# Kernel tuning notes

Hardware: AMD Instinct MI355X
Metric: run time of the kernel (lower is better)

## Reference

```python
import math
import jax, jax.numpy as jnp
import numpy as np

B, D, E, R, TOP_K = 16384, 2048, 64, 128, 2
TAU = 1.0
CAP_FACTOR = 1.25
TOP_C = min(E, max(4, 2 * TOP_K))  # GatingNetwork default top_c


def setup_inputs() -> dict:
    key = jax.random.key(0)
    ks = jax.random.split(key, 7)
    x = jax.random.normal(ks[0], (B, D), dtype=jnp.float32)
    # shared_encoder: nn.Linear(d, d) -> weight [out, in], bias [out]
    We = jax.random.normal(ks[1], (D, D), dtype=jnp.float32) / np.sqrt(D)
    be = jnp.zeros((D,), dtype=jnp.float32)
    # gating: nn.Linear(d, E, bias=False) -> weight [E, d]
    Wg = jax.random.normal(ks[2], (E, D), dtype=jnp.float32) / np.sqrt(D)
    # LowRankExpert per expert: U [r, d], V [d, r], gamma scalar (init 1.0)
    U = jax.random.normal(ks[3], (E, R, D), dtype=jnp.float32) / np.sqrt(D)
    V = jax.random.normal(ks[4], (E, D, R), dtype=jnp.float32) / np.sqrt(R)
    gamma = jnp.ones((E,), dtype=jnp.float32)
    return {"x": x, "We": We, "be": be, "Wg": Wg, "U": U, "V": V, "gamma": gamma}


def reference(x, We, be, Wg, U, V, gamma):
    # shared encoder
    enc = x @ We.T + be  # [B, D]

    # ---- gating: top-C candidates then top-K routing ----
    logits = (enc @ Wg.T) / TAU  # [B, E]
    topc_vals, topc_idx = jax.lax.top_k(logits, TOP_C)          # [B, C]
    topk_vals, pos_in_c = jax.lax.top_k(topc_vals, TOP_K)       # [B, K]
    topk_idx = jnp.take_along_axis(topc_idx, pos_in_c, axis=1)  # [B, K]
    # masked stable softmax over the K selected logits (with 1e-12 eps as in source)
    m = jnp.max(topk_vals, axis=-1, keepdims=True)
    ex = jnp.exp(topk_vals - m)
    w = ex / (jnp.sum(ex, axis=-1, keepdims=True) + 1e-12)      # [B, K]

    # ---- flatten assignments ----
    N = B * TOP_K
    tok = jnp.repeat(jnp.arange(B), TOP_K)   # [N]
    eid = topk_idx.reshape(-1)               # [N]
    wf = w.reshape(-1)                       # [N]
    wmask = wf > 1e-12

    # ---- capacity-based dispatch (sort/group equivalent, fixed shapes) ----
    cap = int(math.ceil(CAP_FACTOR * N / E))  # expert capacity
    onehot = ((eid[:, None] == jnp.arange(E)[None, :]) & wmask[:, None]).astype(jnp.int32)  # [N, E]
    pos = jnp.cumsum(onehot, axis=0) - onehot                      # position within expert
    pos_of = jnp.take_along_axis(pos, eid[:, None], axis=1)[:, 0]  # [N]
    valid = wmask & (pos_of < cap)
    slot = jnp.where(valid, pos_of, cap)  # overflow -> dummy slot (never occurs at this cap)

    # gather tokens to per-expert buffers [E, cap+1, D]
    xbuf = jnp.zeros((E, cap + 1, D), dtype=enc.dtype).at[eid, slot].set(enc[tok])

    # batched low-rank experts: delta = gamma * V @ silu(U @ x)
    h = jax.nn.silu(jnp.einsum('ecd,erd->ecr', xbuf, U))
    delta = jnp.einsum('ecr,edr->ecd', h, V) * gamma[:, None, None]  # [E, cap+1, D]

    # scatter-combine: y = enc + sum_k w_k * delta_k (residual handled since sum w = 1)
    dflat = delta[eid, slot]  # [N, D]
    y = enc.at[tok].add(jnp.where(valid, wf, 0.0)[:, None] * dflat)
    return y
```

## Files before the change

### kernel.cpp

```cpp
#include <hip/hip_runtime.h>
#include <math.h>

#define NTOK 16384
#define DDIM 2048
#define NEXP 64
#define RRANK 128
#define CAP 640

typedef __attribute__((ext_vector_type(8))) short bf16x8;
typedef __attribute__((ext_vector_type(4))) float f32x4;
typedef __attribute__((address_space(1))) const unsigned int gu32_t;
typedef __attribute__((address_space(3))) unsigned int lu32_t;

__device__ __forceinline__ void gload16(const void* g, void* l) {
  __builtin_amdgcn_global_load_lds((gu32_t*)g, (lu32_t*)l, 16, 0, 0);
}

__device__ __forceinline__ float silu_f(float v) {
  return v / (1.f + expf(-v));
}

__device__ __forceinline__ unsigned short f2bf(float f) {
  unsigned int u = __float_as_uint(f);
  unsigned int r = (u + 0x7fffu + ((u >> 16) & 1u)) >> 16;
  return (unsigned short)r;
}

__device__ __forceinline__ float bf2f(unsigned short u) {
  return __uint_as_float(((unsigned int)u) << 16);
}

__device__ __forceinline__ int swz256(int d) {
  return d ^ (((d >> 8) & 7) << 4);
}

__global__ __launch_bounds__(256) void cvt_bf16_kernel(
    const float* __restrict__ in, unsigned short* __restrict__ out, int n4)
{
  int i = blockIdx.x * 256 + threadIdx.x;
  const int stride = gridDim.x * 256;
  for (; i < n4; i += stride) {
    const float4 v = ((const float4*)in)[i];
    ushort4 o;
    o.x = f2bf(v.x); o.y = f2bf(v.y); o.z = f2bf(v.z); o.w = f2bf(v.w);
    ((ushort4*)out)[i] = o;
  }
}

__global__ __launch_bounds__(256) void enc_mfma2(
    const unsigned short* __restrict__ xb, const unsigned short* __restrict__ Web,
    const float* __restrict__ be, float* __restrict__ out)
{
  __shared__ unsigned short At[128 * 32];
  __shared__ unsigned short Bt[128 * 32];
  const int tid = threadIdx.x;
  const int lane = tid & 63, wid = tid >> 6;
  const int wr = wid >> 1, wc = wid & 1;
  const int fr = lane & 15, fq = lane >> 4;
  const int bid = blockIdx.x;
  const int wg = (bid & 7) * 256 + (bid >> 3);
  const int n0 = (wg & 15) * 128, m0 = (wg >> 4) * 128;

  const int doff0 = wid * 1024 + lane * 16;
  const int doff1 = doff0 + 4096;
  const unsigned short* as0 = xb + (size_t)(m0 + (doff0 >> 6)) * DDIM + ((doff0 & 63) >> 1);
  const unsigned short* as1 = xb + (size_t)(m0 + (doff1 >> 6)) * DDIM + ((doff1 & 63) >> 1);
  const unsigned short* bs0 = Web + (size_t)(n0 + (doff0 >> 6)) * DDIM + ((doff0 & 63) >> 1);
  const unsigned short* bs1 = Web + (size_t)(n0 + (doff1 >> 6)) * DDIM + ((doff1 & 63) >> 1);
  char* ad0 = (char*)At + doff0; char* ad1 = (char*)At + doff1;
  char* bd0 = (char*)Bt + doff0; char* bd1 = (char*)Bt + doff1;

  f32x4 acc[4][4];
#pragma unroll
  for (int m = 0; m < 4; ++m)
#pragma unroll
    for (int n = 0; n < 4; ++n) acc[m][n] = (f32x4){0.f, 0.f, 0.f, 0.f};

  for (int kb = 0; kb < DDIM; kb += 32) {
    __syncthreads();
    gload16(as0 + kb, ad0);
    gload16(as1 + kb, ad1);
    gload16(bs0 + kb, bd0);
    gload16(bs1 + kb, bd1);
    __syncthreads();
    bf16x8 af[4], bfr[4];
#pragma unroll
    for (int m = 0; m < 4; ++m)
      af[m] = *(const bf16x8*)&At[(wr * 64 + m * 16 + fr) * 32 + fq * 8];
#pragma unroll
    for (int n = 0; n < 4; ++n)
      bfr[n] = *(const bf16x8*)&Bt[(wc * 64 + n * 16 + fr) * 32 + fq * 8];
#pragma unroll
    for (int m = 0; m < 4; ++m)
#pragma unroll
      for (int n = 0; n < 4; ++n)
        acc[m][n] = __builtin_amdgcn_mfma_f32_16x16x32_bf16(af[m], bfr[n], acc[m][n], 0, 0, 0);
  }

  float bias[4];
#pragma unroll
  for (int n = 0; n < 4; ++n) bias[n] = be[n0 + wc * 64 + n * 16 + fr];
#pragma unroll
  for (int m = 0; m < 4; ++m) {
#pragma unroll
    for (int j = 0; j < 4; ++j) {
      const int row = m0 + wr * 64 + m * 16 + fq * 4 + j;
      float* op = out + (size_t)row * DDIM + n0 + wc * 64 + fr;
#pragma unroll
      for (int n = 0; n < 4; ++n)
        op[n * 16] = acc[m][n][j] + bias[n];
    }
  }
}

__global__ __launch_bounds__(256) void gmat_part_kernel(
    const float* __restrict__ We, const float* __restrict__ Wg,
    double* __restrict__ Gpart)
{
  __shared__ float As[64][68];
  __shared__ float Bs[64][68];
  const int tid = threadIdx.x;
  const int d0 = blockIdx.x * 64;
  const int oc = blockIdx.y;
  const int tx = tid & 15, ty = tid >> 4;
  const int row = tid >> 2, p = (tid & 3) * 16;

  double acc[4][4];
#pragma unroll
  for (int j = 0; j < 4; ++j)
#pragma unroll
    for (int i = 0; i < 4; ++i) acc[j][i] = 0.0;

  for (int o0 = oc * 256; o0 < oc * 256 + 256; o0 += 64) {
    float4 wv[4], gv[4];
#pragma unroll
    for (int q = 0; q < 4; ++q) {
      wv[q] = *(const float4*)(We + (size_t)(o0 + row) * DDIM + d0 + p + q * 4);
      gv[q] = *(const float4*)(Wg + (size_t)row * DDIM + o0 + p + q * 4);
    }
    __syncthreads();
#pragma unroll
    for (int q = 0; q < 4; ++q) {
      const int c = p + q * 4;
      As[row][c + 0] = wv[q].x; As[row][c + 1] = wv[q].y;
      As[row][c + 2] = wv[q].z; As[row][c + 3] = wv[q].w;
      Bs[c + 0][row] = gv[q].x; Bs[c + 1][row] = gv[q].y;
      Bs[c + 2][row] = gv[q].z; Bs[c + 3][row] = gv[q].w;
    }
    __syncthreads();
#pragma unroll 8
    for (int oo = 0; oo < 64; ++oo) {
      double a[4], b[4];
#pragma unroll
      for (int j = 0; j < 4; ++j) a[j] = (double)As[oo][ty * 4 + j];
#pragma unroll
      for (int i = 0; i < 4; ++i) b[i] = (double)Bs[oo][tx * 4 + i];
#pragma unroll
      for (int j = 0; j < 4; ++j)
#pragma unroll
        for (int i = 0; i < 4; ++i)
          acc[j][i] = fma(a[j], b[i], acc[j][i]);
    }
    __syncthreads();
  }
#pragma unroll
  for (int j = 0; j < 4; ++j)
#pragma unroll
    for (int i = 0; i < 4; ++i) {
      const int d = d0 + ty * 4 + j, e = tx * 4 + i;
      Gpart[(size_t)oc * (DDIM * NEXP) + (size_t)e * DDIM + d] = acc[j][i];
    }
}

__global__ __launch_bounds__(256) void greduce_kernel(
    const double* __restrict__ Gpart, double* __restrict__ Gt,
    unsigned short* __restrict__ Gbf)
{
  const int idx = blockIdx.x * 256 + threadIdx.x;
  double s = 0.0;
#pragma unroll
  for (int oc = 0; oc < 8; ++oc)
    s += Gpart[(size_t)oc * (DDIM * NEXP) + idx];
  Gt[idx] = s;
  Gbf[idx] = f2bf((float)s);
}

__global__ __launch_bounds__(256) void bias_c_kernel(
    const float* __restrict__ be, const float* __restrict__ Wg,
    double* __restrict__ c64)
{
  const int e = blockIdx.x;
  const int tid = threadIdx.x;
  double s = 0.0;
  for (int o = tid; o < DDIM; o += 256)
    s += (double)be[o] * (double)Wg[(size_t)e * DDIM + o];
  __shared__ double red[256];
  red[tid] = s;
  __syncthreads();
  for (int st = 128; st > 0; st >>= 1) {
    if (tid < st) red[tid] += red[tid + st];
    __syncthreads();
  }
  if (tid == 0) c64[e] = red[0];
}

__global__ __launch_bounds__(256) void logits_topc_kernel(
    const unsigned short* __restrict__ xb, const unsigned short* __restrict__ Gbf,
    const double* __restrict__ c64, int* __restrict__ cand8)
{
  __shared__ unsigned short At[128 * 32];
  __shared__ unsigned short Bt[64 * 32];
  __shared__ float Ls[128][64];
  const int tid = threadIdx.x;
  const int lane = tid & 63, wid = tid >> 6;
  const int fr = lane & 15, fq = lane >> 4;
  const int t0 = blockIdx.x * 128;

  const int doff0 = wid * 1024 + lane * 16;
  const int doff1 = doff0 + 4096;
  const unsigned short* as0 = xb + (size_t)(t0 + (doff0 >> 6)) * DDIM + ((doff0 & 63) >> 1);
  const unsigned short* as1 = xb + (size_t)(t0 + (doff1 >> 6)) * DDIM + ((doff1 & 63) >> 1);
  const unsigned short* bs0 = Gbf + (size_t)(doff0 >> 6) * DDIM + ((doff0 & 63) >> 1);
  char* ad0 = (char*)At + doff0; char* ad1 = (char*)At + doff1;
  char* bd0 = (char*)Bt + doff0;

  f32x4 acc[2][4];
#pragma unroll
  for (int m = 0; m < 2; ++m)
#pragma unroll
    for (int n = 0; n < 4; ++n) acc[m][n] = (f32x4){0.f, 0.f, 0.f, 0.f};

  for (int kb = 0; kb < DDIM; kb += 32) {
    __syncthreads();
    gload16(as0 + kb, ad0);
    gload16(as1 + kb, ad1);
    gload16(bs0 + kb, bd0);
    __syncthreads();
    bf16x8 af[2], bfr[4];
#pragma unroll
    for (int m = 0; m < 2; ++m)
      af[m] = *(const bf16x8*)&At[(wid * 32 + m * 16 + fr) * 32 + fq * 8];
#pragma unroll
    for (int n = 0; n < 4; ++n)
      bfr[n] = *(const bf16x8*)&Bt[(n * 16 + fr) * 32 + fq * 8];
#pragma unroll
    for (int m = 0; m < 2; ++m)
#pragma unroll
      for (int n = 0; n < 4; ++n)
        acc[m][n] = __builtin_amdgcn_mfma_f32_16x16x32_bf16(af[m], bfr[n], acc[m][n], 0, 0, 0);
  }

#pragma unroll
  for (int m = 0; m < 2; ++m)
#pragma unroll
    for (int j = 0; j < 4; ++j) {
      const int row = wid * 32 + m * 16 + fq * 4 + j;
#pragma unroll
      for (int n = 0; n < 4; ++n)
        Ls[row][n * 16 + fr] = acc[m][n][j];
    }
  __syncthreads();

  if (tid < 128) {
    float v8[8];
    int i8[8];
#pragma unroll
    for (int c = 0; c < 8; ++c) { v8[c] = -INFINITY; i8[c] = 0; }
    for (int e = 0; e < NEXP; ++e) {
      const float v = Ls[tid][e] + (float)c64[e];
      if (v > v8[7]) {
        int p = 7;
        while (p > 0 && v > v8[p - 1]) { v8[p] = v8[p - 1]; i8[p] = i8[p - 1]; --p; }
        v8[p] = v; i8[p] = e;
      }
    }
    int* cp = cand8 + (size_t)(t0 + tid) * 8;
#pragma unroll
    for (int c = 0; c < 8; ++c) cp[c] = i8[c];
  }
}

__global__ __launch_bounds__(256) void refine_kernel(
    const float* __restrict__ x, const double* __restrict__ Gt,
    const double* __restrict__ c64, const int* __restrict__ cand8,
    int* __restrict__ topk, float* __restrict__ wkf)
{
  const int t = blockIdx.x;
  const int tid = threadIdx.x;
  const int lane = tid & 63, w = tid >> 6;
  __shared__ float xs[DDIM];
  __shared__ double red[8][4];

  ((float4*)xs)[tid] = ((const float4*)(x + (size_t)t * DDIM))[tid];
  ((float4*)xs)[tid + 256] = ((const float4*)(x + (size_t)t * DDIM))[tid + 256];
  __syncthreads();

  int myc[8];
#pragma unroll
  for (int c = 0; c < 8; ++c) myc[c] = cand8[(size_t)t * 8 + c];

#pragma unroll
  for (int c = 0; c < 8; ++c) {
    const double* g = Gt + (size_t)myc[c] * DDIM;
    double s = 0.0;
#pragma unroll
    for (int q = 0; q < 8; ++q) {
      const int d = q * 256 + tid;
      s += (double)xs[d] * g[d];
    }
#pragma unroll
    for (int off = 32; off > 0; off >>= 1) s += __shfl_down(s, off);
    if (lane == 0) red[c][w] = s;
  }
  __syncthreads();

  if (tid == 0) {
    double v1 = -1e300, v2 = -1e300;
    int i1 = 0, i2 = 0;
#pragma unroll
    for (int c = 0; c < 8; ++c) {
      const double v = red[c][0] + red[c][1] + red[c][2] + red[c][3] + c64[myc[c]];
      if (v > v1) { v2 = v1; i2 = i1; v1 = v; i1 = myc[c]; }
      else if (v > v2) { v2 = v; i2 = myc[c]; }
    }
    const double e2 = exp(v2 - v1);
    const double s = 1.0 + e2 + 1e-12;
    topk[2 * t] = i1; topk[2 * t + 1] = i2;
    wkf[2 * t] = (float)(1.0 / s);
    wkf[2 * t + 1] = (float)(e2 / s);
  }
}

__global__ __launch_bounds__(256) void route_kernel(
    const int* __restrict__ topk, const float* __restrict__ wkf,
    int* __restrict__ slots , int* __restrict__ counts_eff,
    int* __restrict__ val )
{
  const int e = blockIdx.x;
  const int tid = threadIdx.x;
  const int lane = tid & 63, wave = tid >> 6;
  __shared__ int wcnt[4];
  __shared__ int sbase;
  if (tid == 0) sbase = 0;
  __syncthreads();

  for (int c0 = 0; c0 < NTOK * 2; c0 += 256) {
    const int a = c0 + tid;
    const bool match = (topk[a] == e) && (wkf[a] > 1e-12f);
    const unsigned long long bal = __ballot(match);
    if (lane == 0) wcnt[wave] = __popcll(bal);
    __syncthreads();
    int base = sbase;
    for (int w = 0; w < 4; ++w)
      if (w < wave) base += wcnt[w];
    const int rank = base + (int)__popcll(bal & ((1ull << lane) - 1ull));
    if (match && rank < CAP) {
      slots[e * CAP + rank] = a;
      val[a] = 1;
    }
    __syncthreads();
    if (tid == 0) sbase += wcnt[0] + wcnt[1] + wcnt[2] + wcnt[3];
  }
  __syncthreads();
  if (tid == 0) counts_eff[e] = (sbase < CAP) ? sbase : CAP;
}

__global__ __launch_bounds__(256) void expert_h_mfma(
    const float* __restrict__ enc, const unsigned short* __restrict__ Ub,
    const int* __restrict__ counts_eff, const int* __restrict__ slots,
    unsigned short* __restrict__ Hbuf)
{
  const int lin = blockIdx.x;
  const int wg = (lin & 7) * 80 + (lin >> 3);
  const int e = wg / 10;
  const int t0 = (wg % 10) * 64;
  const int cnt = counts_eff[e];
  if (t0 >= cnt) return;
  __shared__ unsigned short At[64 * 32];
  __shared__ unsigned short Bt[128 * 32];
  __shared__ int toks[64];
  const int tid = threadIdx.x;
  const int lane = tid & 63, wid = tid >> 6;
  const int wr = wid >> 1, wc = wid & 1;
  const int fr = lane & 15, fq = lane >> 4;

  if (tid < 64) {
    const int i = t0 + tid;
    toks[tid] = (i < cnt) ? (slots[e * CAP + i] >> 1) : (slots[e * CAP] >> 1);
  }
  __syncthreads();

  const int arow = tid >> 2, ak0 = (tid & 3) * 8;
  const float* ap = enc + (size_t)toks[arow] * DDIM + ak0;
  unsigned short* awp = &At[arow * 32 + ak0];

  const int doff0 = wid * 1024 + lane * 16;
  const int doff1 = doff0 + 4096;
  const unsigned short* Ue = Ub + (size_t)e * RRANK * DDIM;
  const unsigned short* bsrc0 = Ue + (size_t)(doff0 >> 6) * DDIM + ((doff0 & 63) >> 1);
  const unsigned short* bsrc1 = Ue + (size_t)(doff1 >> 6) * DDIM + ((doff1 & 63) >> 1);
  unsigned short* bdst0 = (unsigned short*)((char*)Bt + doff0);
  unsigned short* bdst1 = (unsigned short*)((char*)Bt + doff1);

  f32x4 acc[2][4];
#pragma unroll
  for (int m = 0; m < 2; ++m)
#pragma unroll
    for (int n = 0; n < 4; ++n) acc[m][n] = (f32x4){0.f, 0.f, 0.f, 0.f};

  float4 a0 = *(const float4*)(ap), a1 = *(const float4*)(ap + 4);

  for (int kb = 0; kb < DDIM; kb += 32) {
    __syncthreads();
    union { unsigned short us[8]; uint4 q; } pk;
    pk.us[0] = f2bf(a0.x); pk.us[1] = f2bf(a0.y);
    pk.us[2] = f2bf(a0.z); pk.us[3] = f2bf(a0.w);
    pk.us[4] = f2bf(a1.x); pk.us[5] = f2bf(a1.y);
    pk.us[6] = f2bf(a1.z); pk.us[7] = f2bf(a1.w);
    *(uint4*)awp = pk.q;
    gload16(bsrc0 + kb, bdst0);
    gload16(bsrc1 + kb, bdst1);
    __syncthreads();
    if (kb + 32 < DDIM) {
      a0 = *(const float4*)(ap + kb + 32);
      a1 = *(const float4*)(ap + kb + 36);
    }
    bf16x8 af[2], bfr[4];
#pragma unroll
    for (int m = 0; m < 2; ++m)
      af[m] = *(const bf16x8*)&At[(wr * 32 + m * 16 + fr) * 32 + fq * 8];
#pragma unroll
    for (int n = 0; n < 4; ++n)
      bfr[n] = *(const bf16x8*)&Bt[(wc * 64 + n * 16 + fr) * 32 + fq * 8];
#pragma unroll
    for (int m = 0; m < 2; ++m)
#pragma unroll
      for (int n = 0; n < 4; ++n)
        acc[m][n] = __builtin_amdgcn_mfma_f32_16x16x32_bf16(af[m], bfr[n], acc[m][n], 0, 0, 0);
  }

#pragma unroll
  for (int m = 0; m < 2; ++m) {
#pragma unroll
    for (int j = 0; j < 4; ++j) {
      const int tl = wr * 32 + m * 16 + fq * 4 + j;
      if (t0 + tl < cnt) {
        unsigned short* hp = Hbuf + (size_t)(e * CAP + t0 + tl) * RRANK + wc * 64 + fr;
#pragma unroll
        for (int n = 0; n < 4; ++n)
          hp[n * 16] = f2bf(silu_f(acc[m][n][j]));
      }
    }
  }
}

__global__ __launch_bounds__(256) void expert_out_mfma(
    const unsigned short* __restrict__ Hbuf, const unsigned short* __restrict__ Vb,
    const float* __restrict__ gamma, const int* __restrict__ counts_eff,
    const int* __restrict__ slots, const float* __restrict__ wkf,
    unsigned short* __restrict__ Dbuf)
{
  const int lin = blockIdx.x;
  const int wg = (lin & 7) * 80 + (lin >> 3);
  const int e = wg / 10;
  const int t0 = (wg % 10) * 64;
  const int cnt = counts_eff[e];
  if (t0 >= cnt) return;
  __shared__ unsigned short Ht[64 * 128];
  __shared__ unsigned short Vt[128 * 128];
  __shared__ int aid[64];
  __shared__ float wts[64];
  const int tid = threadIdx.x;
  const int lane = tid & 63, wid = tid >> 6;
  const int wr = wid >> 1, wc = wid & 1;
  const int fr = lane & 15, fq = lane >> 4;

  if (tid < 64) {
    const int i = t0 + tid;
    if (i < cnt) {
      const int a = slots[e * CAP + i];
      aid[tid] = a;
      wts[tid] = wkf[a] * gamma[e];
    } else { aid[tid] = -1; wts[tid] = 0.f; }
  }

  const unsigned short* hsrc = Hbuf + (size_t)(e * CAP + t0) * RRANK;
  const int hd = wid * 1024 + lane * 16;
#pragma unroll
  for (int is = 0; is < 4; ++is) {
    const int d = is * 4096 + hd;
    gload16(hsrc + (swz256(d) >> 1), (char*)Ht + d);
  }

  const unsigned short* vsrc0 = Vb + (size_t)e * DDIM * RRANK;

  bf16x8 af[2][4];
  float wv[2][4];
  int av[2][4];

  for (int nb = 0; nb < 16; ++nb) {
    __syncthreads();
    const unsigned short* vsrc = vsrc0 + (size_t)nb * 128 * RRANK;
#pragma unroll
    for (int is = 0; is < 8; ++is) {
      const int d = is * 4096 + hd;
      gload16(vsrc + (swz256(d) >> 1), (char*)Vt + d);
    }
    __syncthreads();
    if (nb == 0) {
#pragma unroll
      for (int m = 0; m < 2; ++m) {
        const int row = wr * 32 + m * 16 + fr;
#pragma unroll
        for (int kk = 0; kk < 4; ++kk) {
          const int b = (row * 256 + kk * 64 + fq * 16) ^ ((row & 7) << 4);
          af[m][kk] = *(const bf16x8*)((const char*)Ht + b);
        }
#pragma unroll
        for (int j = 0; j < 4; ++j) {
          const int tl = wr * 32 + m * 16 + fq * 4 + j;
          wv[m][j] = wts[tl];
          av[m][j] = (t0 + tl < cnt) ? aid[tl] : -1;
        }
      }
    }

    f32x4 acc[2][4];
#pragma unroll
    for (int m = 0; m < 2; ++m)
#pragma unroll
      for (int n = 0; n < 4; ++n) acc[m][n] = (f32x4){0.f, 0.f, 0.f, 0.f};

#pragma unroll
    for (int n = 0; n < 4; ++n) {
      const int drow = wc * 64 + n * 16 + fr;
#pragma unroll
      for (int kk = 0; kk < 4; ++kk) {
        const int b = (drow * 256 + kk * 64 + fq * 16) ^ ((drow & 7) << 4);
        const bf16x8 bfr = *(const bf16x8*)((const char*)Vt + b);
#pragma unroll
        for (int m = 0; m < 2; ++m)
          acc[m][n] = __builtin_amdgcn_mfma_f32_16x16x32_bf16(af[m][kk], bfr, acc[m][n], 0, 0, 0);
      }
    }

#pragma unroll
    for (int m = 0; m < 2; ++m) {
#pragma unroll
      for (int j = 0; j < 4; ++j) {
        if (av[m][j] >= 0) {
          const float w = wv[m][j];
          unsigned short* dp = Dbuf + (size_t)av[m][j] * DDIM + nb * 128 + wc * 64 + fr;
#pragma unroll
          for (int n = 0; n < 4; ++n)
            dp[n * 16] = f2bf(acc[m][n][j] * w);
        }
      }
    }
  }
}

__global__ __launch_bounds__(256) void combine_kernel(
    const unsigned short* __restrict__ Dbuf, const int* __restrict__ val,
    float* __restrict__ y)
{
  const int t = blockIdx.x;
  const int tid = threadIdx.x;
  const int c0 = tid * 8;
  float* yp = y + (size_t)t * DDIM + c0;
  const int v0 = val[2 * t], v1 = val[2 * t + 1];

  float4 o0 = *(const float4*)(yp);
  float4 o1 = *(const float4*)(yp + 4);
  float o[8] = {o0.x, o0.y, o0.z, o0.w, o1.x, o1.y, o1.z, o1.w};

  if (v0) {
    const ushort4 d0 = *(const ushort4*)(Dbuf + (size_t)(2 * t) * DDIM + c0);
    const ushort4 d1 = *(const ushort4*)(Dbuf + (size_t)(2 * t) * DDIM + c0 + 4);
    o[0] += bf2f(d0.x); o[1] += bf2f(d0.y); o[2] += bf2f(d0.z); o[3] += bf2f(d0.w);
    o[4] += bf2f(d1.x); o[5] += bf2f(d1.y); o[6] += bf2f(d1.z); o[7] += bf2f(d1.w);
  }
  if (v1) {
    const ushort4 d0 = *(const ushort4*)(Dbuf + (size_t)(2 * t + 1) * DDIM + c0);
    const ushort4 d1 = *(const ushort4*)(Dbuf + (size_t)(2 * t + 1) * DDIM + c0 + 4);
    o[0] += bf2f(d0.x); o[1] += bf2f(d0.y); o[2] += bf2f(d0.z); o[3] += bf2f(d0.w);
    o[4] += bf2f(d1.x); o[5] += bf2f(d1.y); o[6] += bf2f(d1.z); o[7] += bf2f(d1.w);
  }
  *(float4*)(yp) = (float4){o[0], o[1], o[2], o[3]};
  *(float4*)(yp + 4) = (float4){o[4], o[5], o[6], o[7]};
}

extern "C" void kernel_launch(void* const* d_in, const int* in_sizes, int n_in,
                              void* d_out, int out_size, void* d_ws, size_t ws_size,
                              hipStream_t stream)
{
  const float* x     = (const float*)d_in[0];
  const float* We    = (const float*)d_in[1];
  const float* be    = (const float*)d_in[2];
  const float* Wg    = (const float*)d_in[3];
  const float* U     = (const float*)d_in[4];
  const float* V     = (const float*)d_in[5];
  const float* gamma = (const float*)d_in[6];
  float* y = (float*)d_out;

  char* ws = (char*)d_ws;
  int*            topk       = (int*)(ws + 0);
  float*          wkf        = (float*)(ws + 131072);
  int*            counts_eff = (int*)(ws + 262144);
  double*         c64        = (double*)(ws + 262400);
  int*            cand8      = (int*)(ws + 262912);
  double*         Gt         = (double*)(ws + 787200);
  unsigned short* G_bf       = (unsigned short*)(ws + 1835776);
  int*            slots      = (int*)(ws + 2097920);
  int*            val        = (int*)(ws + 2261760);
  double*         Gpart      = (double*)(ws + 2392832);
  unsigned short* x_bf       = (unsigned short*)(ws + 10781952);
  unsigned short* We_bf      = (unsigned short*)(ws + 77890816);
  unsigned short* U_bf       = (unsigned short*)(ws + 86279424);
  unsigned short* V_bf       = (unsigned short*)(ws + 119833856);
  unsigned short* Hbuf       = (unsigned short*)(ws + 153388288);
  unsigned short* Dbuf       = (unsigned short*)(ws + 163874048);

  hipMemsetAsync(val, 0, 131072, stream);

  cvt_bf16_kernel<<<dim3(2048), 256, 0, stream>>>(x, x_bf, NTOK * DDIM / 4);
  cvt_bf16_kernel<<<dim3(2048), 256, 0, stream>>>(We, We_bf, DDIM * DDIM / 4);
  cvt_bf16_kernel<<<dim3(2048), 256, 0, stream>>>(U, U_bf, NEXP * RRANK * DDIM / 4);
  cvt_bf16_kernel<<<dim3(2048), 256, 0, stream>>>(V, V_bf, NEXP * DDIM * RRANK / 4);

  gmat_part_kernel<<<dim3(32, 8), 256, 0, stream>>>(We, Wg, Gpart);
  greduce_kernel<<<dim3(512), 256, 0, stream>>>(Gpart, Gt, G_bf);
  bias_c_kernel<<<dim3(64), 256, 0, stream>>>(be, Wg, c64);
  logits_topc_kernel<<<dim3(128), 256, 0, stream>>>(x_bf, G_bf, c64, cand8);
  refine_kernel<<<dim3(NTOK), 256, 0, stream>>>(x, Gt, c64, cand8, topk, wkf);
  route_kernel<<<dim3(64), 256, 0, stream>>>(topk, wkf, slots, counts_eff, val);

  enc_mfma2<<<dim3(2048), 256, 0, stream>>>(x_bf, We_bf, be, y);
  expert_h_mfma<<<dim3(640), 256, 0, stream>>>(y, U_bf, counts_eff, slots, Hbuf);
  expert_out_mfma<<<dim3(640), 256, 0, stream>>>(Hbuf, V_bf, gamma, counts_eff, slots, wkf, Dbuf);
  combine_kernel<<<dim3(NTOK), 256, 0, stream>>>(Dbuf, val, y);
}
```

Before: 806.0 us.

## Fuse expert kernels, widen encoder K tile with swizzle, merge bf16 conversions

Merges the four fp32-to-bf16 conversion launches into one kernel. The encoder GEMM now uses a 64-wide K tile with an XOR-swizzled LDS layout and also writes a bf16 copy of enc. The two expert GEMMs are fused into one kernel that keeps the SiLU hidden activations in LDS and gathers bf16 encodings with direct-to-LDS loads. This removes the Hbuf round trip, per-iteration fp32-to-bf16 conversion and extra launches, at the cost of an extra bf16 enc write and more LDS per block.

```diff
diff --git a/kernel.cpp b/kernel.cpp
--- a/kernel.cpp
+++ b/kernel.cpp
@@ -34,25 +34,38 @@
   return d ^ (((d >> 8) & 7) << 4);
 }
 
-__global__ __launch_bounds__(256) void cvt_bf16_kernel(
-    const float* __restrict__ in, unsigned short* __restrict__ out, int n4)
-{
+__global__ __launch_bounds__(256) void cvt_all_kernel(
+    const float* __restrict__ x, const float* __restrict__ We,
+    const float* __restrict__ U, const float* __restrict__ V,
+    unsigned short* __restrict__ xb, unsigned short* __restrict__ Web,
+    unsigned short* __restrict__ Ub, unsigned short* __restrict__ Vb)
+{
+  const int S0 = NTOK * DDIM / 4;
+  const int S1 = DDIM * DDIM / 4;
+  const int S2 = NEXP * RRANK * DDIM / 4;
+  const int total = S0 + S1 + 2 * S2;
   int i = blockIdx.x * 256 + threadIdx.x;
   const int stride = gridDim.x * 256;
-  for (; i < n4; i += stride) {
-    const float4 v = ((const float4*)in)[i];
+  for (; i < total; i += stride) {
+    const float* in; unsigned short* out; int j;
+    if (i < S0) { in = x; out = xb; j = i; }
+    else if (i < S0 + S1) { in = We; out = Web; j = i - S0; }
+    else if (i < S0 + S1 + S2) { in = U; out = Ub; j = i - S0 - S1; }
+    else { in = V; out = Vb; j = i - S0 - S1 - S2; }
+    const float4 v = ((const float4*)in)[j];
     ushort4 o;
     o.x = f2bf(v.x); o.y = f2bf(v.y); o.z = f2bf(v.z); o.w = f2bf(v.w);
-    ((ushort4*)out)[i] = o;
-  }
-}
-
-__global__ __launch_bounds__(256) void enc_mfma2(
+    ((ushort4*)out)[j] = o;
+  }
+}
+
+__global__ __launch_bounds__(256) void enc_mfma3(
     const unsigned short* __restrict__ xb, const unsigned short* __restrict__ Web,
-    const float* __restrict__ be, float* __restrict__ out)
-{
-  __shared__ unsigned short At[128 * 32];
-  __shared__ unsigned short Bt[128 * 32];
+    const float* __restrict__ be, float* __restrict__ out,
+    unsigned short* __restrict__ encbf)
+{
+  __shared__ unsigned short At[128 * 64];
+  __shared__ unsigned short Bt[128 * 64];
   const int tid = threadIdx.x;
   const int lane = tid & 63, wid = tid >> 6;
   const int wr = wid >> 1, wc = wid & 1;
@@ -61,14 +74,20 @@
   const int wg = (bid & 7) * 256 + (bid >> 3);
   const int n0 = (wg & 15) * 128, m0 = (wg >> 4) * 128;
 
-  const int doff0 = wid * 1024 + lane * 16;
-  const int doff1 = doff0 + 4096;
-  const unsigned short* as0 = xb + (size_t)(m0 + (doff0 >> 6)) * DDIM + ((doff0 & 63) >> 1);
-  const unsigned short* as1 = xb + (size_t)(m0 + (doff1 >> 6)) * DDIM + ((doff1 & 63) >> 1);
-  const unsigned short* bs0 = Web + (size_t)(n0 + (doff0 >> 6)) * DDIM + ((doff0 & 63) >> 1);
-  const unsigned short* bs1 = Web + (size_t)(n0 + (doff1 >> 6)) * DDIM + ((doff1 & 63) >> 1);
-  char* ad0 = (char*)At + doff0; char* ad1 = (char*)At + doff1;
-  char* bd0 = (char*)Bt + doff0; char* bd1 = (char*)Bt + doff1;
+  const unsigned short* asrc[4];
+  const unsigned short* bsrc[4];
+  char* adst[4];
+  char* bdst[4];
+#pragma unroll
+  for (int is = 0; is < 4; ++is) {
+    const int doff = is * 4096 + tid * 16;
+    const int r = doff >> 7;
+    const int cs = ((doff >> 4) & 7) ^ (r & 7);
+    asrc[is] = xb + (size_t)(m0 + r) * DDIM + cs * 8;
+    bsrc[is] = Web + (size_t)(n0 + r) * DDIM + cs * 8;
+    adst[is] = (char*)At + doff;
+    bdst[is] = (char*)Bt + doff;
+  }
 
   f32x4 acc[4][4];
 #pragma unroll
@@ -76,25 +95,35 @@
 #pragma unroll
     for (int n = 0; n < 4; ++n) acc[m][n] = (f32x4){0.f, 0.f, 0.f, 0.f};
 
-  for (int kb = 0; kb < DDIM; kb += 32) {
-    __syncthreads();
-    gload16(as0 + kb, ad0);
-    gload16(as1 + kb, ad1);
-    gload16(bs0 + kb, bd0);
-    gload16(bs1 + kb, bd1);
-    __syncthreads();
-    bf16x8 af[4], bfr[4];
-#pragma unroll
-    for (int m = 0; m < 4; ++m)
-      af[m] = *(const bf16x8*)&At[(wr * 64 + m * 16 + fr) * 32 + fq * 8];
-#pragma unroll
-    for (int n = 0; n < 4; ++n)
-      bfr[n] = *(const bf16x8*)&Bt[(wc * 64 + n * 16 + fr) * 32 + fq * 8];
-#pragma unroll
-    for (int m = 0; m < 4; ++m)
-#pragma unroll
-      for (int n = 0; n < 4; ++n)
-        acc[m][n] = __builtin_amdgcn_mfma_f32_16x16x32_bf16(af[m], bfr[n], acc[m][n], 0, 0, 0);
+  for (int kb = 0; kb < DDIM; kb += 64) {
+    __syncthreads();
+#pragma unroll
+    for (int is = 0; is < 4; ++is) {
+      gload16(asrc[is] + kb, adst[is]);
+      gload16(bsrc[is] + kb, bdst[is]);
+    }
+    __syncthreads();
+#pragma unroll
+    for (int kk = 0; kk < 2; ++kk) {
+      bf16x8 af[4], bfv[4];
+#pragma unroll
+      for (int m = 0; m < 4; ++m) {
+        const int row = wr * 64 + m * 16 + fr;
+        af[m] = *(const bf16x8*)((const char*)At +
+                 row * 128 + (((kk * 4 + fq) ^ (row & 7)) << 4));
+      }
+#pragma unroll
+      for (int n = 0; n < 4; ++n) {
+        const int row = wc * 64 + n * 16 + fr;
+        bfv[n] = *(const bf16x8*)((const char*)Bt +
+                  row * 128 + (((kk * 4 + fq) ^ (row & 7)) << 4));
+      }
+#pragma unroll
+      for (int m = 0; m < 4; ++m)
+#pragma unroll
+        for (int n = 0; n < 4; ++n)
+          acc[m][n] = __builtin_amdgcn_mfma_f32_16x16x32_bf16(af[m], bfv[n], acc[m][n], 0, 0, 0);
+    }
   }
 
   float bias[4];
@@ -105,10 +134,15 @@
 #pragma unroll
     for (int j = 0; j < 4; ++j) {
       const int row = m0 + wr * 64 + m * 16 + fq * 4 + j;
-      float* op = out + (size_t)row * DDIM + n0 + wc * 64 + fr;
-#pragma unroll
-      for (int n = 0; n < 4; ++n)
-        op[n * 16] = acc[m][n][j] + bias[n];
+      const size_t base = (size_t)row * DDIM + n0 + wc * 64 + fr;
+      float* op = out + base;
+      unsigned short* ob = encbf + base;
+#pragma unroll
+      for (int n = 0; n < 4; ++n) {
+        const float v = acc[m][n][j] + bias[n];
+        op[n * 16] = v;
+        ob[n * 16] = f2bf(v);
+      }
     }
   }
 }
@@ -365,10 +399,11 @@
   if (tid == 0) counts_eff[e] = (sbase < CAP) ? sbase : CAP;
 }
 
-__global__ __launch_bounds__(256) void expert_h_mfma(
-    const float* __restrict__ enc, const unsigned short* __restrict__ Ub,
+__global__ __launch_bounds__(256) void expert_fused(
+    const unsigned short* __restrict__ encbf, const unsigned short* __restrict__ Ub,
+    const unsigned short* __restrict__ Vb, const float* __restrict__ gamma,
     const int* __restrict__ counts_eff, const int* __restrict__ slots,
-    unsigned short* __restrict__ Hbuf)
+    const float* __restrict__ wkf, unsigned short* __restrict__ Dbuf)
 {
   const int lin = blockIdx.x;
   const int wg = (lin & 7) * 80 + (lin >> 3);
@@ -376,100 +411,13 @@
   const int t0 = (wg % 10) * 64;
   const int cnt = counts_eff[e];
   if (t0 >= cnt) return;
-  __shared__ unsigned short At[64 * 32];
-  __shared__ unsigned short Bt[128 * 32];
+
+  __shared__ int aid[64];
   __shared__ int toks[64];
-  const int tid = threadIdx.x;
-  const int lane = tid & 63, wid = tid >> 6;
-  const int wr = wid >> 1, wc = wid & 1;
-  const int fr = lane & 15, fq = lane >> 4;
-
-  if (tid < 64) {
-    const int i = t0 + tid;
-    toks[tid] = (i < cnt) ? (slots[e * CAP + i] >> 1) : (slots[e * CAP] >> 1);
-  }
-  __syncthreads();
-
-  const int arow = tid >> 2, ak0 = (tid & 3) * 8;
-  const float* ap = enc + (size_t)toks[arow] * DDIM + ak0;
-  unsigned short* awp = &At[arow * 32 + ak0];
-
-  const int doff0 = wid * 1024 + lane * 16;
-  const int doff1 = doff0 + 4096;
-  const unsigned short* Ue = Ub + (size_t)e * RRANK * DDIM;
-  const unsigned short* bsrc0 = Ue + (size_t)(doff0 >> 6) * DDIM + ((doff0 & 63) >> 1);
-  const unsigned short* bsrc1 = Ue + (size_t)(doff1 >> 6) * DDIM + ((doff1 & 63) >> 1);
-  unsigned short* bdst0 = (unsigned short*)((char*)Bt + doff0);
-  unsigned short* bdst1 = (unsigned short*)((char*)Bt + doff1);
-
-  f32x4 acc[2][4];
-#pragma unroll
-  for (int m = 0; m < 2; ++m)
-#pragma unroll
-    for (int n = 0; n < 4; ++n) acc[m][n] = (f32x4){0.f, 0.f, 0.f, 0.f};
-
-  float4 a0 = *(const float4*)(ap), a1 = *(const float4*)(ap + 4);
-
-  for (int kb = 0; kb < DDIM; kb += 32) {
-    __syncthreads();
-    union { unsigned short us[8]; uint4 q; } pk;
-    pk.us[0] = f2bf(a0.x); pk.us[1] = f2bf(a0.y);
-    pk.us[2] = f2bf(a0.z); pk.us[3] = f2bf(a0.w);
-    pk.us[4] = f2bf(a1.x); pk.us[5] = f2bf(a1.y);
-    pk.us[6] = f2bf(a1.z); pk.us[7] = f2bf(a1.w);
-    *(uint4*)awp = pk.q;
-    gload16(bsrc0 + kb, bdst0);
-    gload16(bsrc1 + kb, bdst1);
-    __syncthreads();
-    if (kb + 32 < DDIM) {
-      a0 = *(const float4*)(ap + kb + 32);
-      a1 = *(const float4*)(ap + kb + 36);
-    }
-    bf16x8 af[2], bfr[4];
-#pragma unroll
-    for (int m = 0; m < 2; ++m)
-      af[m] = *(const bf16x8*)&At[(wr * 32 + m * 16 + fr) * 32 + fq * 8];
-#pragma unroll
-    for (int n = 0; n < 4; ++n)
-      bfr[n] = *(const bf16x8*)&Bt[(wc * 64 + n * 16 + fr) * 32 + fq * 8];
-#pragma unroll
-    for (int m = 0; m < 2; ++m)
-#pragma unroll
-      for (int n = 0; n < 4; ++n)
-        acc[m][n] = __builtin_amdgcn_mfma_f32_16x16x32_bf16(af[m], bfr[n], acc[m][n], 0, 0, 0);
-  }
-
-#pragma unroll
-  for (int m = 0; m < 2; ++m) {
-#pragma unroll
-    for (int j = 0; j < 4; ++j) {
-      const int tl = wr * 32 + m * 16 + fq * 4 + j;
-      if (t0 + tl < cnt) {
-        unsigned short* hp = Hbuf + (size_t)(e * CAP + t0 + tl) * RRANK + wc * 64 + fr;
-#pragma unroll
-        for (int n = 0; n < 4; ++n)
-          hp[n * 16] = f2bf(silu_f(acc[m][n][j]));
-      }
-    }
-  }
-}
-
-__global__ __launch_bounds__(256) void expert_out_mfma(
-    const unsigned short* __restrict__ Hbuf, const unsigned short* __restrict__ Vb,
-    const float* __restrict__ gamma, const int* __restrict__ counts_eff,
-    const int* __restrict__ slots, const float* __restrict__ wkf,
-    unsigned short* __restrict__ Dbuf)
-{
-  const int lin = blockIdx.x;
-  const int wg = (lin & 7) * 80 + (lin >> 3);
-  const int e = wg / 10;
-  const int t0 = (wg % 10) * 64;
-  const int cnt = counts_eff[e];
-  if (t0 >= cnt) return;
+  __shared__ float wts[64];
   __shared__ unsigned short Ht[64 * 128];
-  __shared__ unsigned short Vt[128 * 128];
-  __shared__ int aid[64];
-  __shared__ float wts[64];
+  __shared__ char U2[32768];
+
   const int tid = threadIdx.x;
   const int lane = tid & 63, wid = tid >> 6;
   const int wr = wid >> 1, wc = wid & 1;
@@ -480,50 +428,124 @@
     if (i < cnt) {
       const int a = slots[e * CAP + i];
       aid[tid] = a;
+      toks[tid] = a >> 1;
       wts[tid] = wkf[a] * gamma[e];
-    } else { aid[tid] = -1; wts[tid] = 0.f; }
-  }
-
-  const unsigned short* hsrc = Hbuf + (size_t)(e * CAP + t0) * RRANK;
-  const int hd = wid * 1024 + lane * 16;
+    } else {
+      aid[tid] = -1;
+      toks[tid] = slots[e * CAP] >> 1;
+      wts[tid] = 0.f;
+    }
+  }
+  __syncthreads();
+
+  unsigned short* At = (unsigned short*)U2;
+  unsigned short* Bt = (unsigned short*)(U2 + 8192);
+  const unsigned short* Ue = Ub + (size_t)e * RRANK * DDIM;
+
+  size_t aoff[2]; char* adst[2];
+#pragma unroll
+  for (int is = 0; is < 2; ++is) {
+    const int doff = is * 4096 + tid * 16;
+    const int r = doff >> 7;
+    const int cs = ((doff >> 4) & 7) ^ (r & 7);
+    aoff[is] = (size_t)toks[r] * DDIM + cs * 8;
+    adst[is] = (char*)At + doff;
+  }
+  const unsigned short* bsrc[4]; char* bdst[4];
 #pragma unroll
   for (int is = 0; is < 4; ++is) {
-    const int d = is * 4096 + hd;
-    gload16(hsrc + (swz256(d) >> 1), (char*)Ht + d);
-  }
-
-  const unsigned short* vsrc0 = Vb + (size_t)e * DDIM * RRANK;
-
-  bf16x8 af[2][4];
+    const int doff = is * 4096 + tid * 16;
+    const int r = doff >> 7;
+    const int cs = ((doff >> 4) & 7) ^ (r & 7);
+    bsrc[is] = Ue + (size_t)r * DDIM + cs * 8;
+    bdst[is] = (char*)Bt + doff;
+  }
+
+  f32x4 hacc[2][4];
+#pragma unroll
+  for (int m = 0; m < 2; ++m)
+#pragma unroll
+    for (int n = 0; n < 4; ++n) hacc[m][n] = (f32x4){0.f, 0.f, 0.f, 0.f};
+
+  for (int kb = 0; kb < DDIM; kb += 64) {
+    __syncthreads();
+    gload16(encbf + aoff[0] + kb, adst[0]);
+    gload16(encbf + aoff[1] + kb, adst[1]);
+#pragma unroll
+    for (int is = 0; is < 4; ++is)
+      gload16(bsrc[is] + kb, bdst[is]);
+    __syncthreads();
+#pragma unroll
+    for (int kk = 0; kk < 2; ++kk) {
+      bf16x8 af[2], bfv[4];
+#pragma unroll
+      for (int m = 0; m < 2; ++m) {
+        const int row = wr * 32 + m * 16 + fr;
+        af[m] = *(const bf16x8*)((const char*)At +
+                 row * 128 + (((kk * 4 + fq) ^ (row & 7)) << 4));
+      }
+#pragma unroll
+      for (int n = 0; n < 4; ++n) {
+        const int row = wc * 64 + n * 16 + fr;
+        bfv[n] = *(const bf16x8*)((const char*)Bt +
+                  row * 128 + (((kk * 4 + fq) ^ (row & 7)) << 4));
+      }
+#pragma unroll
+      for (int m = 0; m < 2; ++m)
+#pragma unroll
+        for (int n = 0; n < 4; ++n)
+          hacc[m][n] = __builtin_amdgcn_mfma_f32_16x16x32_bf16(af[m], bfv[n], hacc[m][n], 0, 0, 0);
+    }
+  }
+
+  __syncthreads();
+#pragma unroll
+  for (int m = 0; m < 2; ++m) {
+#pragma unroll
+    for (int j = 0; j < 4; ++j) {
+      const int row = wr * 32 + m * 16 + fq * 4 + j;
+#pragma unroll
+      for (int n = 0; n < 4; ++n) {
+        const int col = wc * 64 + n * 16 + fr;
+        const int b = (row * 256 + col * 2) ^ ((row & 7) << 4);
+        *(unsigned short*)((char*)Ht + b) = f2bf(silu_f(hacc[m][n][j]));
+      }
+    }
+  }
+  __syncthreads();
+
+  unsigned short* Vt = (unsigned short*)U2;
+  const unsigned short* Ve = Vb + (size_t)e * DDIM * RRANK;
+  const int hd = tid * 16;
+
+  bf16x8 paf[2][4];
   float wv[2][4];
   int av[2][4];
+#pragma unroll
+  for (int m = 0; m < 2; ++m) {
+    const int row = wr * 32 + m * 16 + fr;
+#pragma unroll
+    for (int kk = 0; kk < 4; ++kk) {
+      const int b = (row * 256 + kk * 64 + fq * 16) ^ ((row & 7) << 4);
+      paf[m][kk] = *(const bf16x8*)((const char*)Ht + b);
+    }
+#pragma unroll
+    for (int j = 0; j < 4; ++j) {
+      const int tl = wr * 32 + m * 16 + fq * 4 + j;
+      wv[m][j] = wts[tl];
+      av[m][j] = aid[tl];
+    }
+  }
 
   for (int nb = 0; nb < 16; ++nb) {
     __syncthreads();
-    const unsigned short* vsrc = vsrc0 + (size_t)nb * 128 * RRANK;
+    const unsigned short* vsrc = Ve + (size_t)nb * 128 * RRANK;
 #pragma unroll
     for (int is = 0; is < 8; ++is) {
       const int d = is * 4096 + hd;
       gload16(vsrc + (swz256(d) >> 1), (char*)Vt + d);
     }
     __syncthreads();
-    if (nb == 0) {
-#pragma unroll
-      for (int m = 0; m < 2; ++m) {
-        const int row = wr * 32 + m * 16 + fr;
-#pragma unroll
-        for (int kk = 0; kk < 4; ++kk) {
-          const int b = (row * 256 + kk * 64 + fq * 16) ^ ((row & 7) << 4);
-          af[m][kk] = *(const bf16x8*)((const char*)Ht + b);
-        }
-#pragma unroll
-        for (int j = 0; j < 4; ++j) {
-          const int tl = wr * 32 + m * 16 + fq * 4 + j;
-          wv[m][j] = wts[tl];
-          av[m][j] = (t0 + tl < cnt) ? aid[tl] : -1;
-        }
-      }
-    }
 
     f32x4 acc[2][4];
 #pragma unroll
@@ -540,7 +562,7 @@
         const bf16x8 bfr = *(const bf16x8*)((const char*)Vt + b);
 #pragma unroll
         for (int m = 0; m < 2; ++m)
-          acc[m][n] = __builtin_amdgcn_mfma_f32_16x16x32_bf16(af[m][kk], bfr, acc[m][n], 0, 0, 0);
+          acc[m][n] = __builtin_amdgcn_mfma_f32_16x16x32_bf16(paf[m][kk], bfr, acc[m][n], 0, 0, 0);
       }
     }
 
@@ -613,20 +635,17 @@
   unsigned short* G_bf       = (unsigned short*)(ws + 1835776);
   int*            slots      = (int*)(ws + 2097920);
   int*            val        = (int*)(ws + 2261760);
-  double*         Gpart      = (double*)(ws + 2392832);
-  unsigned short* x_bf       = (unsigned short*)(ws + 10781952);
-  unsigned short* We_bf      = (unsigned short*)(ws + 77890816);
-  unsigned short* U_bf       = (unsigned short*)(ws + 86279424);
-  unsigned short* V_bf       = (unsigned short*)(ws + 119833856);
-  unsigned short* Hbuf       = (unsigned short*)(ws + 153388288);
-  unsigned short* Dbuf       = (unsigned short*)(ws + 163874048);
+  unsigned short* Dbuf       = (unsigned short*)(ws + 2392832);
+  unsigned short* x_bf       = (unsigned short*)(ws + 2392832);
+  unsigned short* We_bf      = (unsigned short*)(ws + 69501696);
+  double*         Gpart      = (double*)(ws + 77890304);
+  unsigned short* U_bf       = (unsigned short*)(ws + 136610560);
+  unsigned short* V_bf       = (unsigned short*)(ws + 170164992);
+  unsigned short* enc_bf     = (unsigned short*)(ws + 203719424);
 
   hipMemsetAsync(val, 0, 131072, stream);
 
-  cvt_bf16_kernel<<<dim3(2048), 256, 0, stream>>>(x, x_bf, NTOK * DDIM / 4);
-  cvt_bf16_kernel<<<dim3(2048), 256, 0, stream>>>(We, We_bf, DDIM * DDIM / 4);
-  cvt_bf16_kernel<<<dim3(2048), 256, 0, stream>>>(U, U_bf, NEXP * RRANK * DDIM / 4);
-  cvt_bf16_kernel<<<dim3(2048), 256, 0, stream>>>(V, V_bf, NEXP * DDIM * RRANK / 4);
+  cvt_all_kernel<<<dim3(2048), 256, 0, stream>>>(x, We, U, V, x_bf, We_bf, U_bf, V_bf);
 
   gmat_part_kernel<<<dim3(32, 8), 256, 0, stream>>>(We, Wg, Gpart);
   greduce_kernel<<<dim3(512), 256, 0, stream>>>(Gpart, Gt, G_bf);
@@ -635,8 +654,7 @@
   refine_kernel<<<dim3(NTOK), 256, 0, stream>>>(x, Gt, c64, cand8, topk, wkf);
   route_kernel<<<dim3(64), 256, 0, stream>>>(topk, wkf, slots, counts_eff, val);
 
-  enc_mfma2<<<dim3(2048), 256, 0, stream>>>(x_bf, We_bf, be, y);
-  expert_h_mfma<<<dim3(640), 256, 0, stream>>>(y, U_bf, counts_eff, slots, Hbuf);
-  expert_out_mfma<<<dim3(640), 256, 0, stream>>>(Hbuf, V_bf, gamma, counts_eff, slots, wkf, Dbuf);
+  enc_mfma3<<<dim3(2048), 256, 0, stream>>>(x_bf, We_bf, be, y, enc_bf);
+  expert_fused<<<dim3(640), 256, 0, stream>>>(enc_bf, U_bf, V_bf, gamma, counts_eff, slots, wkf, Dbuf);
   combine_kernel<<<dim3(NTOK), 256, 0, stream>>>(Dbuf, val, y);
 }
```

Result: no change. 796.5 us (-1.2%).
